# Performance work log

Measured on AMD Instinct MI355X. Metric: run time of the kernel, lower is better.

## Reference

```python
import jax, jax.numpy as jnp
import numpy as np

N_NODES = 100000
N_EDGES = 800000
N_REL = 16
D = 64
EPS = 1e-12
NEG_SLOPE = 0.01  # nn.LeakyReLU default


def _l2norm(x):
    # matches torch F.normalize(p=2, dim=-1)
    n = jnp.sqrt(jnp.sum(x * x, axis=-1, keepdims=True))
    return x / jnp.maximum(n, EPS)


def setup_inputs() -> dict:
    key = jax.random.key(0)
    ks = jax.random.split(key, 12)
    inp = {
        "src": jax.random.randint(ks[0], (N_EDGES,), 0, N_NODES, dtype=jnp.int32),
        "dst": jax.random.randint(ks[1], (N_EDGES,), 0, N_NODES, dtype=jnp.int32),
        "etype": jax.random.randint(ks[2], (N_EDGES,), 0, N_REL, dtype=jnp.int32),
        "ent_embed": jax.random.normal(ks[3], (N_NODES, D), jnp.float32) * 0.1,
        "ent_transfer": jax.random.normal(ks[4], (N_NODES, D), jnp.float32) * 0.1,
        "rel_embed": jax.random.normal(ks[5], (N_REL, D), jnp.float32) * 0.1,
        "rel_transfer": jax.random.normal(ks[6], (N_REL, D), jnp.float32) * 0.1,
        "W1_0": jax.random.normal(ks[7], (64, 32), jnp.float32) * (1.0 / np.sqrt(64)),
        "b1_0": jnp.zeros((32,), jnp.float32),
        "W2_0": jax.random.normal(ks[8], (64, 32), jnp.float32) * (1.0 / np.sqrt(64)),
        "b2_0": jnp.zeros((32,), jnp.float32),
        "W1_1": jax.random.normal(ks[9], (32, 16), jnp.float32) * (1.0 / np.sqrt(32)),
        "b1_1": jnp.zeros((16,), jnp.float32),
        "W2_1": jax.random.normal(ks[10], (32, 16), jnp.float32) * (1.0 / np.sqrt(32)),
        "b2_1": jnp.zeros((16,), jnp.float32),
    }
    return inp


def _compute_att(src, dst, etype, ent_embed, ent_transfer, rel_embed, rel_transfer):
    # per-edge gathers: h = dst node, t = src node (KGAT att_score convention)
    h_e = ent_embed[dst]          # [E, D]
    t_e = ent_embed[src]          # [E, D]
    h_p = ent_transfer[dst]
    t_p = ent_transfer[src]
    r_p = rel_transfer[etype]     # [E, D]
    r_e = rel_embed[etype]        # [E, D]
    # TransD projection + L2 normalize
    Mrt = _l2norm(t_e + jnp.sum(t_e * t_p, -1, keepdims=True) * r_p)
    Mrh = _l2norm(h_e + jnp.sum(h_e * h_p, -1, keepdims=True) * r_p)
    att = jnp.sum(Mrt * jnp.tanh(Mrh + r_e), axis=-1)  # [E]
    # edge softmax grouped by destination node
    m = jax.ops.segment_max(att, dst, num_segments=N_NODES)
    m = jnp.where(jnp.isfinite(m), m, 0.0)
    ex = jnp.exp(att - m[dst])
    s = jax.ops.segment_sum(ex, dst, num_segments=N_NODES)
    return ex / jnp.maximum(s[dst], EPS)  # [E]


def _bi_layer(node, N_h, W1, b1, W2, b2):
    out1 = jax.nn.leaky_relu((node + N_h) @ W1 + b1, NEG_SLOPE)
    out2 = jax.nn.leaky_relu((node * N_h) @ W2 + b2, NEG_SLOPE)
    return out1 + out2


def reference(src, dst, etype, ent_embed, ent_transfer, rel_embed, rel_transfer,
              W1_0, b1_0, W2_0, b2_0, W1_1, b1_1, W2_1, b2_1):
    att = _compute_att(src, dst, etype, ent_embed, ent_transfer, rel_embed, rel_transfer)
    node = ent_embed
    all_embed = [node]
    for (W1, b1, W2, b2) in [(W1_0, b1_0, W2_0, b2_0), (W1_1, b1_1, W2_1, b2_1)]:
        # u_mul_e + sum: N_h[v] = sum_{e: dst(e)=v} att_e * node[src(e)]
        msg = att[:, None] * node[src]                      # [E, d]
        N_h = jax.ops.segment_sum(msg, dst, num_segments=N_NODES)
        node = _bi_layer(node, N_h, W1, b1, W2, b2)         # dropout p=0 (eval)
        all_embed.append(_l2norm(node))
    return jnp.concatenate(all_embed, axis=1)  # [N, 64+32+16]
```

## Files before the change

kernel.cpp:

```cpp
#include <hip/hip_runtime.h>
#include <math.h>

#define EPSF 1e-12f
#define LOG2E 1.44269504f

__device__ __forceinline__ float red16(float v) {
    v += __shfl_xor(v, 1, 16);
    v += __shfl_xor(v, 2, 16);
    v += __shfl_xor(v, 4, 16);
    v += __shfl_xor(v, 8, 16);
    return v;
}

__device__ __forceinline__ float red8(float v) {
    v += __shfl_xor(v, 1, 8);
    v += __shfl_xor(v, 2, 8);
    v += __shfl_xor(v, 4, 8);
    return v;
}

__device__ __forceinline__ float fast_tanh(float x) {
    float E = __builtin_amdgcn_exp2f(x * (2.0f * LOG2E));
    return 1.0f - 2.0f * __builtin_amdgcn_rcpf(E + 1.0f);
}

__device__ __forceinline__ float inv_norm(float x) {
    return __builtin_amdgcn_rsqf(fmaxf(x, 1e-24f));
}

__device__ __forceinline__ float leaky(float x) {
    return x > 0.0f ? x : 0.01f * x;
}

__global__ __launch_bounds__(256) void prep(
    const float* __restrict__ ent, const float* __restrict__ entT,
    float* __restrict__ dot, const int* __restrict__ dst,
    int* __restrict__ deg, int N16, int E) {
    int gid = blockIdx.x * 256 + threadIdx.x;
    if (gid < N16) {
        int v = gid >> 4, lane = gid & 15;
        const float4 a = *(const float4*)(ent  + (size_t)v * 64 + lane * 4);
        const float4 b = *(const float4*)(entT + (size_t)v * 64 + lane * 4);
        float d = red16(a.x*b.x + a.y*b.y + a.z*b.z + a.w*b.w);
        if (lane == 0) dot[v] = d;
    } else {
        int e = gid - N16;
        if (e < E) atomicAdd(&deg[dst[e]], 1);
    }
}


__global__ __launch_bounds__(256) void scan_reduce(
    const int* __restrict__ deg, int* __restrict__ part, int N) {
    __shared__ int sh[256];
    int t = threadIdx.x, i = blockIdx.x * 256 + t;
    sh[t] = (i < N) ? deg[i] : 0;
    __syncthreads();
    for (int off = 128; off > 0; off >>= 1) {
        if (t < off) sh[t] += sh[t + off];
        __syncthreads();
    }
    if (t == 0) part[blockIdx.x] = sh[0];
}

__global__ __launch_bounds__(1024) void scan_part(int* __restrict__ part, int nb) {
    __shared__ int sh[1024];
    int t = threadIdx.x;
    int x = (t < nb) ? part[t] : 0;
    sh[t] = x;
    __syncthreads();
    for (int off = 1; off < 1024; off <<= 1) {
        int y = (t >= off) ? sh[t - off] : 0;
        __syncthreads();
        sh[t] += y;
        __syncthreads();
    }
    if (t < nb) part[t] = sh[t] - x;
}

__global__ __launch_bounds__(256) void scan_write(
    int* __restrict__ rowptr, const int* __restrict__ part, int N) {
    __shared__ int sh[256];
    int t = threadIdx.x, i = blockIdx.x * 256 + t;
    int x = (i < N) ? rowptr[i] : 0;
    sh[t] = x;
    __syncthreads();
    for (int off = 1; off < 256; off <<= 1) {
        int y = (t >= off) ? sh[t - off] : 0;
        __syncthreads();
        sh[t] += y;
        __syncthreads();
    }
    if (i < N) rowptr[i] = part[blockIdx.x] + sh[t] - x;
}

__global__ __launch_bounds__(256) void scatter_edges(
    const int* __restrict__ src, const int* __restrict__ dst,
    const int* __restrict__ ety, int* __restrict__ rowptr,
    int* __restrict__ spk, int E) {
    int e = blockIdx.x * 256 + threadIdx.x;
    if (e < E) {
        int slot = atomicAdd(&rowptr[dst[e]], 1);
        spk[slot] = src[e] | (ety[e] << 20);
    }
}

__global__ __launch_bounds__(256) void fused_l0(
    const int* __restrict__ rowptr, const int* __restrict__ spk,
    const float* __restrict__ ent, const float* __restrict__ dot,
    const float* __restrict__ relE, const float* __restrict__ relT,
    const float* __restrict__ W1, const float* __restrict__ b1,
    const float* __restrict__ W2, const float* __restrict__ b2,
    float* __restrict__ exatt, float* __restrict__ sinv,
    float* __restrict__ node1raw, float* __restrict__ out, int N) {
    __shared__ float al[8][68];
    __shared__ float bl[8][68];
    __shared__ float rT[16][68];
    __shared__ float rE[16][68];
    int t = threadIdx.x;

    {
        int r = t >> 4, c = (t & 15) * 4;
        *(float4*)&rT[r][c] = *(const float4*)(relT + r * 64 + c);
        *(float4*)&rE[r][c] = *(const float4*)(relE + r * 64 + c);
    }
    __syncthreads();

    int nv = t >> 5, half = (t >> 4) & 1, lane = t & 15;
    int v = blockIdx.x * 8 + nv;
    if (v >= N) return;

    int s = v ? rowptr[v - 1] : 0;
    int epos = rowptr[v];
    int deg = epos - s;
    int mid = s + ((deg + 1) >> 1);
    int hs   = half ? mid  : s;
    int hend = half ? epos : mid;

    const float4 he = *(const float4*)(ent + (size_t)v * 64 + lane * 4);
    float dh = dot[v];

    float4 macc = {0.f, 0.f, 0.f, 0.f};
    float sumex = 0.0f;

    for (int base = hs; base < hend; base += 16) {
        int rem = hend - base;
        int cnt = rem < 16 ? rem : 16;
        int mypk = spk[base + (lane < rem ? lane : rem - 1)];

        int pk0 = __shfl(mypk, 0, 16);
        int pk1 = __shfl(mypk, cnt > 1 ? 1 : 0, 16);
        float4 te0 = *(const float4*)(ent + (size_t)(pk0 & 0xFFFFF) * 64 + lane * 4);
        float  sd0 = dot[pk0 & 0xFFFFF];
        float4 te1 = *(const float4*)(ent + (size_t)(pk1 & 0xFFFFF) * 64 + lane * 4);
        float  sd1 = dot[pk1 & 0xFFFFF];

        for (int k = 0; k < cnt; k += 2) {
            float4 ta = te0, tb = te1;
            float  sa = sd0, sb = sd1;
            int rva = (pk0 >> 20) & 15;
            int rvb = (pk1 >> 20) & 15;
            bool hasb = (k + 1) < cnt;

            if (k + 2 < cnt) {
                pk0 = __shfl(mypk, k + 2, 16);
                pk1 = __shfl(mypk, (k + 3 < cnt) ? (k + 3) : (k + 2), 16);
                te0 = *(const float4*)(ent + (size_t)(pk0 & 0xFFFFF) * 64 + lane * 4);
                sd0 = dot[pk0 & 0xFFFFF];
                te1 = *(const float4*)(ent + (size_t)(pk1 & 0xFFFFF) * 64 + lane * 4);
                sd1 = dot[pk1 & 0xFFFFF];
            }

            const float4 rpa = *(const float4*)&rT[rva][lane * 4];
            const float4 rea = *(const float4*)&rE[rva][lane * 4];
            const float4 rpb = *(const float4*)&rT[rvb][lane * 4];
            const float4 reb = *(const float4*)&rE[rvb][lane * 4];

            float4 mta, mha, mtb, mhb;
            mta.x = ta.x + sa * rpa.x; mta.y = ta.y + sa * rpa.y;
            mta.z = ta.z + sa * rpa.z; mta.w = ta.w + sa * rpa.w;
            mha.x = he.x + dh * rpa.x; mha.y = he.y + dh * rpa.y;
            mha.z = he.z + dh * rpa.z; mha.w = he.w + dh * rpa.w;
            mtb.x = tb.x + sb * rpb.x; mtb.y = tb.y + sb * rpb.y;
            mtb.z = tb.z + sb * rpb.z; mtb.w = tb.w + sb * rpb.w;
            mhb.x = he.x + dh * rpb.x; mhb.y = he.y + dh * rpb.y;
            mhb.z = he.z + dh * rpb.z; mhb.w = he.w + dh * rpb.w;

            float ssta = red16(mta.x*mta.x + mta.y*mta.y + mta.z*mta.z + mta.w*mta.w);
            float ssha = red16(mha.x*mha.x + mha.y*mha.y + mha.z*mha.z + mha.w*mha.w);
            float sstb = red16(mtb.x*mtb.x + mtb.y*mtb.y + mtb.z*mtb.z + mtb.w*mtb.w);
            float sshb = red16(mhb.x*mhb.x + mhb.y*mhb.y + mhb.z*mhb.z + mhb.w*mhb.w);
            float ita = inv_norm(ssta), iha = inv_norm(ssha);
            float itb = inv_norm(sstb), ihb = inv_norm(sshb);

            float txa = fast_tanh(mha.x * iha + rea.x);
            float tya = fast_tanh(mha.y * iha + rea.y);
            float tza = fast_tanh(mha.z * iha + rea.z);
            float twa = fast_tanh(mha.w * iha + rea.w);
            float txb = fast_tanh(mhb.x * ihb + reb.x);
            float tyb = fast_tanh(mhb.y * ihb + reb.y);
            float tzb = fast_tanh(mhb.z * ihb + reb.z);
            float twb = fast_tanh(mhb.w * ihb + reb.w);

            float atta = ita * red16(mta.x*txa + mta.y*tya + mta.z*tza + mta.w*twa);
            float attb = itb * red16(mtb.x*txb + mtb.y*tyb + mtb.z*tzb + mtb.w*twb);

            float exa  = __builtin_amdgcn_exp2f(atta * LOG2E);
            float exbR = __builtin_amdgcn_exp2f(attb * LOG2E);
            float exb  = hasb ? exbR : 0.0f;

            if (lane == 0) {
                exatt[base + k] = exa;
                if (hasb) exatt[base + k + 1] = exbR;
            }
            sumex += exa + exb;
            macc.x += exa * ta.x + exb * tb.x;
            macc.y += exa * ta.y + exb * tb.y;
            macc.z += exa * ta.z + exb * tb.z;
            macc.w += exa * ta.w + exb * tb.w;
        }
    }

    sumex  += __shfl_xor(sumex,  16, 32);
    macc.x += __shfl_xor(macc.x, 16, 32);
    macc.y += __shfl_xor(macc.y, 16, 32);
    macc.z += __shfl_xor(macc.z, 16, 32);
    macc.w += __shfl_xor(macc.w, 16, 32);

    float inv = 1.0f / fmaxf(sumex, EPSF);
    if ((t & 31) == 0) sinv[v] = inv;
    macc.x *= inv; macc.y *= inv; macc.z *= inv; macc.w *= inv;

    if (!half) {
        *(float4*)(out + (size_t)v * 112 + lane * 4) = he;
        float4 av, bv;
        av.x = he.x + macc.x; av.y = he.y + macc.y;
        av.z = he.z + macc.z; av.w = he.w + macc.w;
        bv.x = he.x * macc.x; bv.y = he.y * macc.y;
        bv.z = he.z * macc.z; bv.w = he.w * macc.w;
        *(float4*)&al[nv][lane * 4] = av;
        *(float4*)&bl[nv][lane * 4] = bv;
    }

    int j = t & 31;
    float acc1 = b1[j], acc2 = b2[j];
    #pragma unroll
    for (int d = 0; d < 64; d += 4) {
        float4 a4 = *(const float4*)&al[nv][d];
        float4 b4 = *(const float4*)&bl[nv][d];
        acc1 += a4.x * W1[(d+0)*32 + j] + a4.y * W1[(d+1)*32 + j]
              + a4.z * W1[(d+2)*32 + j] + a4.w * W1[(d+3)*32 + j];
        acc2 += b4.x * W2[(d+0)*32 + j] + b4.y * W2[(d+1)*32 + j]
              + b4.z * W2[(d+2)*32 + j] + b4.w * W2[(d+3)*32 + j];
    }
    node1raw[(size_t)v * 32 + j] = leaky(acc1) + leaky(acc2);
}

__global__ __launch_bounds__(256) void fused_l1(
    const int* __restrict__ rowptr, const int* __restrict__ spk,
    const float* __restrict__ exatt, const float* __restrict__ sinv,
    const float* __restrict__ node1raw,
    const float* __restrict__ W1, const float* __restrict__ b1,
    const float* __restrict__ W2, const float* __restrict__ b2,
    float* __restrict__ out, int N) {
    __shared__ float A[16][36];
    __shared__ float B[16][36];
    int t = threadIdx.x;
    int nv = t >> 4, half = (t >> 3) & 1, lane = t & 7;
    int v = blockIdx.x * 16 + nv;
    if (v >= N) return;

    int s = v ? rowptr[v - 1] : 0;
    int epos = rowptr[v];
    int deg = epos - s;
    int mid = s + ((deg + 1) >> 1);
    int hs   = half ? mid  : s;
    int hend = half ? epos : mid;

    float4 n = *(const float4*)(node1raw + (size_t)v * 32 + lane * 4);
    float4 acc = {0.f, 0.f, 0.f, 0.f};

    for (int base = hs; base < hend; base += 8) {
        int rem = hend - base;
        int cnt = rem < 8 ? rem : 8;
        int idx = base + (lane < rem ? lane : rem - 1);
        int   mypk = spk[idx];
        float myex = exatt[idx];

        int pk0 = __shfl(mypk, 0, 8);
        int pk1 = __shfl(mypk, cnt > 1 ? 1 : 0, 8);
        float4 x0 = *(const float4*)(node1raw + (size_t)(pk0 & 0xFFFFF) * 32 + lane * 4);
        float4 x1 = *(const float4*)(node1raw + (size_t)(pk1 & 0xFFFFF) * 32 + lane * 4);

        for (int k = 0; k < cnt; k += 2) {
            float4 xa = x0, xb = x1;
            float aa = __shfl(myex, k, 8);
            float ab = __shfl(myex, (k + 1 < cnt) ? (k + 1) : k, 8);
            if (!((k + 1) < cnt)) ab = 0.0f;

            if (k + 2 < cnt) {
                pk0 = __shfl(mypk, k + 2, 8);
                pk1 = __shfl(mypk, (k + 3 < cnt) ? (k + 3) : (k + 2), 8);
                x0 = *(const float4*)(node1raw + (size_t)(pk0 & 0xFFFFF) * 32 + lane * 4);
                x1 = *(const float4*)(node1raw + (size_t)(pk1 & 0xFFFFF) * 32 + lane * 4);
            }
            acc.x += aa * xa.x + ab * xb.x;
            acc.y += aa * xa.y + ab * xb.y;
            acc.z += aa * xa.z + ab * xb.z;
            acc.w += aa * xa.w + ab * xb.w;
        }
    }
    acc.x += __shfl_xor(acc.x, 8, 16);
    acc.y += __shfl_xor(acc.y, 8, 16);
    acc.z += __shfl_xor(acc.z, 8, 16);
    acc.w += __shfl_xor(acc.w, 8, 16);

    float inv = sinv[v];
    acc.x *= inv; acc.y *= inv; acc.z *= inv; acc.w *= inv;

    float ss = red8(n.x*n.x + n.y*n.y + n.z*n.z + n.w*n.w);
    float inv1 = inv_norm(ss);

    if (!half) {
        float4 nn = {n.x*inv1, n.y*inv1, n.z*inv1, n.w*inv1};
        *(float4*)(out + (size_t)v * 112 + 64 + lane * 4) = nn;
        float4 av = {n.x + acc.x, n.y + acc.y, n.z + acc.z, n.w + acc.w};
        float4 bv = {n.x * acc.x, n.y * acc.y, n.z * acc.z, n.w * acc.w};
        *(float4*)&A[nv][lane * 4] = av;
        *(float4*)&B[nv][lane * 4] = bv;
    }

    int j = t & 15;
    float a1 = b1[j], a2 = b2[j];
    #pragma unroll
    for (int d = 0; d < 32; d += 4) {
        float4 a4 = *(const float4*)&A[nv][d];
        float4 b4 = *(const float4*)&B[nv][d];
        a1 += a4.x * W1[(d+0)*16 + j] + a4.y * W1[(d+1)*16 + j]
            + a4.z * W1[(d+2)*16 + j] + a4.w * W1[(d+3)*16 + j];
        a2 += b4.x * W2[(d+0)*16 + j] + b4.y * W2[(d+1)*16 + j]
            + b4.z * W2[(d+2)*16 + j] + b4.w * W2[(d+3)*16 + j];
    }
    float tot = leaky(a1) + leaky(a2);
    float s2 = red16(tot * tot);
    float inv2 = inv_norm(s2);
    out[(size_t)v * 112 + 96 + j] = tot * inv2;
}

extern "C" void kernel_launch(void* const* d_in, const int* in_sizes, int n_in,
                              void* d_out, int out_size, void* d_ws, size_t ws_size,
                              hipStream_t stream) {
    const int*   src  = (const int*)d_in[0];
    const int*   dst  = (const int*)d_in[1];
    const int*   ety  = (const int*)d_in[2];
    const float* ent  = (const float*)d_in[3];
    const float* entT = (const float*)d_in[4];
    const float* relE = (const float*)d_in[5];
    const float* relT = (const float*)d_in[6];
    const float* W1_0 = (const float*)d_in[7];
    const float* b1_0 = (const float*)d_in[8];
    const float* W2_0 = (const float*)d_in[9];
    const float* b2_0 = (const float*)d_in[10];
    const float* W1_1 = (const float*)d_in[11];
    const float* b1_1 = (const float*)d_in[12];
    const float* W2_1 = (const float*)d_in[13];
    const float* b2_1 = (const float*)d_in[14];
    float* out = (float*)d_out;

    const int E = in_sizes[0];
    const int N = in_sizes[3] / 64;
    const int nb = (N + 255) / 256;

    auto al256 = [](size_t x) { return (x + 255) & ~(size_t)255; };
    char* ws = (char*)d_ws;
    size_t offExatt = 0;
    size_t offS     = al256(offExatt + (size_t)E * 4);
    size_t offDot   = al256(offS + (size_t)N * 4);
    size_t offRow   = al256(offDot + (size_t)N * 4);
    size_t offSpk   = al256(offRow + (size_t)N * 4);
    size_t offPart  = al256(offSpk + (size_t)E * 4);
    size_t offN1    = al256(offPart + (size_t)nb * 4);
    float* exatt    = (float*)(ws + offExatt);
    float* sinv     = (float*)(ws + offS);
    float* dot      = (float*)(ws + offDot);
    int*   rowptr   = (int*)(ws + offRow);
    int*   spk      = (int*)(ws + offSpk);
    int*   part     = (int*)(ws + offPart);
    float* node1raw = (float*)(ws + offN1);

    hipMemsetAsync(rowptr, 0, (size_t)N * 4, stream);
    int N16 = N * 16;
    prep<<<(N16 + E + 255) / 256, 256, 0, stream>>>(ent, entT, dot, dst,
                                                    rowptr, N16, E);
    scan_reduce<<<nb, 256, 0, stream>>>(rowptr, part, N);
    scan_part<<<1, 1024, 0, stream>>>(part, nb);
    scan_write<<<nb, 256, 0, stream>>>(rowptr, part, N);
    int blkE = (E + 255) / 256;
    scatter_edges<<<blkE, 256, 0, stream>>>(src, dst, ety, rowptr, spk, E);

    fused_l0<<<(N + 7) / 8, 256, 0, stream>>>(
        rowptr, spk, ent, dot, relE, relT,
        W1_0, b1_0, W2_0, b2_0, exatt, sinv, node1raw, out, N);

    fused_l1<<<(N + 15) / 16, 256, 0, stream>>>(
        rowptr, spk, exatt, sinv, node1raw,
        W1_1, b1_1, W2_1, b2_1, out, N);
}
```

Measured before the change: 231.0 us.

## Pack src dot into edge list, use DPP reductions, stage transposed weights in LDS

The scatter step now stores each edge's source dot product next to its packed src/etype as an int2, so fused_l0 no longer does a dependent random gather of dot per edge. Shuffle-based row reductions become DPP row ops. The per-edge exp values are gathered into one lane each and written as a single coalesced store per chunk instead of serial lane-0 stores. Both MLP stages load transposed weights into LDS as float4 once per block, and the LDS padding is removed. The cost is a wider edge array (more bytes written in scatter and read in fused_l1), possible LDS bank conflicts from the removed padding, and the assumption that DPP row controls match the old xor masks.

Result: faster. 210.3 us (-9.0%).

```diff
diff --git a/kernel.cpp b/kernel.cpp
--- a/kernel.cpp
+++ b/kernel.cpp
@@ -4,19 +4,24 @@
 #define EPSF 1e-12f
 #define LOG2E 1.44269504f
 
+template <int CTRL>
+__device__ __forceinline__ float dppadd(float x) {
+    union { float f; int i; } u, r;
+    u.f = x;
+    r.i = __builtin_amdgcn_update_dpp(0, u.i, CTRL, 0xF, 0xF, false);
+    return x + r.f;
+}
 __device__ __forceinline__ float red16(float v) {
-    v += __shfl_xor(v, 1, 16);
-    v += __shfl_xor(v, 2, 16);
-    v += __shfl_xor(v, 4, 16);
-    v += __shfl_xor(v, 8, 16);
+    v = dppadd<0xB1>(v); v = dppadd<0x4E>(v);
+    v = dppadd<0x141>(v); v = dppadd<0x140>(v);
     return v;
 }
-
 __device__ __forceinline__ float red8(float v) {
-    v += __shfl_xor(v, 1, 8);
-    v += __shfl_xor(v, 2, 8);
-    v += __shfl_xor(v, 4, 8);
+    v = dppadd<0xB1>(v); v = dppadd<0x4E>(v); v = dppadd<0x141>(v);
     return v;
+}
+__device__ __forceinline__ float xor8add(float v) {
+    return dppadd<0x128>(v);
 }
 
 __device__ __forceinline__ float fast_tanh(float x) {
@@ -96,33 +101,44 @@
 
 __global__ __launch_bounds__(256) void scatter_edges(
     const int* __restrict__ src, const int* __restrict__ dst,
-    const int* __restrict__ ety, int* __restrict__ rowptr,
-    int* __restrict__ spk, int E) {
+    const int* __restrict__ ety, const float* __restrict__ dot,
+    int* __restrict__ rowptr, int2* __restrict__ spk2, int E) {
     int e = blockIdx.x * 256 + threadIdx.x;
     if (e < E) {
+        int sv = src[e];
         int slot = atomicAdd(&rowptr[dst[e]], 1);
-        spk[slot] = src[e] | (ety[e] << 20);
+        spk2[slot] = make_int2(sv | (ety[e] << 20), __float_as_int(dot[sv]));
     }
 }
 
 __global__ __launch_bounds__(256) void fused_l0(
-    const int* __restrict__ rowptr, const int* __restrict__ spk,
+    const int* __restrict__ rowptr, const int2* __restrict__ spk2,
     const float* __restrict__ ent, const float* __restrict__ dot,
     const float* __restrict__ relE, const float* __restrict__ relT,
     const float* __restrict__ W1, const float* __restrict__ b1,
     const float* __restrict__ W2, const float* __restrict__ b2,
     float* __restrict__ exatt, float* __restrict__ sinv,
     float* __restrict__ node1raw, float* __restrict__ out, int N) {
-    __shared__ float al[8][68];
-    __shared__ float bl[8][68];
-    __shared__ float rT[16][68];
-    __shared__ float rE[16][68];
+    __shared__ float  al[8][64];
+    __shared__ float  bl[8][64];
+    __shared__ float  rT[16][64];
+    __shared__ float  rE[16][64];
+    __shared__ float4 WtA[16 * 32];
+    __shared__ float4 WtB[16 * 32];
     int t = threadIdx.x;
 
     {
         int r = t >> 4, c = (t & 15) * 4;
         *(float4*)&rT[r][c] = *(const float4*)(relT + r * 64 + c);
         *(float4*)&rE[r][c] = *(const float4*)(relE + r * 64 + c);
+        int j = t & 31;
+        for (int dd = t >> 5; dd < 16; dd += 8) {
+            int d4 = dd * 4;
+            WtA[dd * 32 + j] = make_float4(W1[(d4+0)*32 + j], W1[(d4+1)*32 + j],
+                                           W1[(d4+2)*32 + j], W1[(d4+3)*32 + j]);
+            WtB[dd * 32 + j] = make_float4(W2[(d4+0)*32 + j], W2[(d4+1)*32 + j],
+                                           W2[(d4+2)*32 + j], W2[(d4+3)*32 + j]);
+        }
     }
     __syncthreads();
 
@@ -146,14 +162,15 @@
     for (int base = hs; base < hend; base += 16) {
         int rem = hend - base;
         int cnt = rem < 16 ? rem : 16;
-        int mypk = spk[base + (lane < rem ? lane : rem - 1)];
-
-        int pk0 = __shfl(mypk, 0, 16);
-        int pk1 = __shfl(mypk, cnt > 1 ? 1 : 0, 16);
+        int2 ms = spk2[base + (lane < rem ? lane : rem - 1)];
+        float myex = 0.0f;
+
+        int pk0 = __shfl(ms.x, 0, 16);
+        int pk1 = __shfl(ms.x, cnt > 1 ? 1 : 0, 16);
+        float sd0 = __int_as_float(__shfl(ms.y, 0, 16));
+        float sd1 = __int_as_float(__shfl(ms.y, cnt > 1 ? 1 : 0, 16));
         float4 te0 = *(const float4*)(ent + (size_t)(pk0 & 0xFFFFF) * 64 + lane * 4);
-        float  sd0 = dot[pk0 & 0xFFFFF];
         float4 te1 = *(const float4*)(ent + (size_t)(pk1 & 0xFFFFF) * 64 + lane * 4);
-        float  sd1 = dot[pk1 & 0xFFFFF];
 
         for (int k = 0; k < cnt; k += 2) {
             float4 ta = te0, tb = te1;
@@ -163,12 +180,13 @@
             bool hasb = (k + 1) < cnt;
 
             if (k + 2 < cnt) {
-                pk0 = __shfl(mypk, k + 2, 16);
-                pk1 = __shfl(mypk, (k + 3 < cnt) ? (k + 3) : (k + 2), 16);
+                int i2 = k + 2, i3 = (k + 3 < cnt) ? (k + 3) : (k + 2);
+                pk0 = __shfl(ms.x, i2, 16);
+                pk1 = __shfl(ms.x, i3, 16);
+                sd0 = __int_as_float(__shfl(ms.y, i2, 16));
+                sd1 = __int_as_float(__shfl(ms.y, i3, 16));
                 te0 = *(const float4*)(ent + (size_t)(pk0 & 0xFFFFF) * 64 + lane * 4);
-                sd0 = dot[pk0 & 0xFFFFF];
                 te1 = *(const float4*)(ent + (size_t)(pk1 & 0xFFFFF) * 64 + lane * 4);
-                sd1 = dot[pk1 & 0xFFFFF];
             }
 
             const float4 rpa = *(const float4*)&rT[rva][lane * 4];
@@ -209,16 +227,16 @@
             float exbR = __builtin_amdgcn_exp2f(attb * LOG2E);
             float exb  = hasb ? exbR : 0.0f;
 
-            if (lane == 0) {
-                exatt[base + k] = exa;
-                if (hasb) exatt[base + k + 1] = exbR;
-            }
+            myex = (lane == k) ? exa : myex;
+            myex = (lane == k + 1) ? exbR : myex;
+
             sumex += exa + exb;
             macc.x += exa * ta.x + exb * tb.x;
             macc.y += exa * ta.y + exb * tb.y;
             macc.z += exa * ta.z + exb * tb.z;
             macc.w += exa * ta.w + exb * tb.w;
         }
+        if (lane < cnt) exatt[base + lane] = myex;
     }
 
     sumex  += __shfl_xor(sumex,  16, 32);
@@ -245,27 +263,41 @@
     int j = t & 31;
     float acc1 = b1[j], acc2 = b2[j];
     #pragma unroll
-    for (int d = 0; d < 64; d += 4) {
-        float4 a4 = *(const float4*)&al[nv][d];
-        float4 b4 = *(const float4*)&bl[nv][d];
-        acc1 += a4.x * W1[(d+0)*32 + j] + a4.y * W1[(d+1)*32 + j]
-              + a4.z * W1[(d+2)*32 + j] + a4.w * W1[(d+3)*32 + j];
-        acc2 += b4.x * W2[(d+0)*32 + j] + b4.y * W2[(d+1)*32 + j]
-              + b4.z * W2[(d+2)*32 + j] + b4.w * W2[(d+3)*32 + j];
+    for (int dd = 0; dd < 16; ++dd) {
+        float4 a4 = *(const float4*)&al[nv][dd * 4];
+        float4 b4 = *(const float4*)&bl[nv][dd * 4];
+        float4 wa = WtA[dd * 32 + j];
+        float4 wb = WtB[dd * 32 + j];
+        acc1 += a4.x*wa.x + a4.y*wa.y + a4.z*wa.z + a4.w*wa.w;
+        acc2 += b4.x*wb.x + b4.y*wb.y + b4.z*wb.z + b4.w*wb.w;
     }
     node1raw[(size_t)v * 32 + j] = leaky(acc1) + leaky(acc2);
 }
 
 __global__ __launch_bounds__(256) void fused_l1(
-    const int* __restrict__ rowptr, const int* __restrict__ spk,
+    const int* __restrict__ rowptr, const int2* __restrict__ spk2,
     const float* __restrict__ exatt, const float* __restrict__ sinv,
     const float* __restrict__ node1raw,
     const float* __restrict__ W1, const float* __restrict__ b1,
     const float* __restrict__ W2, const float* __restrict__ b2,
     float* __restrict__ out, int N) {
-    __shared__ float A[16][36];
-    __shared__ float B[16][36];
+    __shared__ float  A[16][32];
+    __shared__ float  B[16][32];
+    __shared__ float4 WtC[8 * 16];
+    __shared__ float4 WtD[8 * 16];
     int t = threadIdx.x;
+
+    {
+        int tt = t & 127;
+        int j = tt & 15, dd = tt >> 4;
+        int d4 = dd * 4;
+        const float* W = (t < 128) ? W1 : W2;
+        float4* Wt = (t < 128) ? WtC : WtD;
+        Wt[dd * 16 + j] = make_float4(W[(d4+0)*16 + j], W[(d4+1)*16 + j],
+                                      W[(d4+2)*16 + j], W[(d4+3)*16 + j]);
+    }
+    __syncthreads();
+
     int nv = t >> 4, half = (t >> 3) & 1, lane = t & 7;
     int v = blockIdx.x * 16 + nv;
     if (v >= N) return;
@@ -284,7 +316,7 @@
         int rem = hend - base;
         int cnt = rem < 8 ? rem : 8;
         int idx = base + (lane < rem ? lane : rem - 1);
-        int   mypk = spk[idx];
+        int   mypk = spk2[idx].x;
         float myex = exatt[idx];
 
         int pk0 = __shfl(mypk, 0, 8);
@@ -310,10 +342,10 @@
             acc.w += aa * xa.w + ab * xb.w;
         }
     }
-    acc.x += __shfl_xor(acc.x, 8, 16);
-    acc.y += __shfl_xor(acc.y, 8, 16);
-    acc.z += __shfl_xor(acc.z, 8, 16);
-    acc.w += __shfl_xor(acc.w, 8, 16);
+    acc.x = xor8add(acc.x);
+    acc.y = xor8add(acc.y);
+    acc.z = xor8add(acc.z);
+    acc.w = xor8add(acc.w);
 
     float inv = sinv[v];
     acc.x *= inv; acc.y *= inv; acc.z *= inv; acc.w *= inv;
@@ -333,13 +365,13 @@
     int j = t & 15;
     float a1 = b1[j], a2 = b2[j];
     #pragma unroll
-    for (int d = 0; d < 32; d += 4) {
-        float4 a4 = *(const float4*)&A[nv][d];
-        float4 b4 = *(const float4*)&B[nv][d];
-        a1 += a4.x * W1[(d+0)*16 + j] + a4.y * W1[(d+1)*16 + j]
-            + a4.z * W1[(d+2)*16 + j] + a4.w * W1[(d+3)*16 + j];
-        a2 += b4.x * W2[(d+0)*16 + j] + b4.y * W2[(d+1)*16 + j]
-            + b4.z * W2[(d+2)*16 + j] + b4.w * W2[(d+3)*16 + j];
+    for (int dd = 0; dd < 8; ++dd) {
+        float4 a4 = *(const float4*)&A[nv][dd * 4];
+        float4 b4 = *(const float4*)&B[nv][dd * 4];
+        float4 wc = WtC[dd * 16 + j];
+        float4 wd = WtD[dd * 16 + j];
+        a1 += a4.x*wc.x + a4.y*wc.y + a4.z*wc.z + a4.w*wc.w;
+        a2 += b4.x*wd.x + b4.y*wd.y + b4.z*wd.z + b4.w*wd.w;
     }
     float tot = leaky(a1) + leaky(a2);
     float s2 = red16(tot * tot);
@@ -378,13 +410,13 @@
     size_t offDot   = al256(offS + (size_t)N * 4);
     size_t offRow   = al256(offDot + (size_t)N * 4);
     size_t offSpk   = al256(offRow + (size_t)N * 4);
-    size_t offPart  = al256(offSpk + (size_t)E * 4);
+    size_t offPart  = al256(offSpk + (size_t)E * 8);
     size_t offN1    = al256(offPart + (size_t)nb * 4);
     float* exatt    = (float*)(ws + offExatt);
     float* sinv     = (float*)(ws + offS);
     float* dot      = (float*)(ws + offDot);
     int*   rowptr   = (int*)(ws + offRow);
-    int*   spk      = (int*)(ws + offSpk);
+    int2*  spk2     = (int2*)(ws + offSpk);
     int*   part     = (int*)(ws + offPart);
     float* node1raw = (float*)(ws + offN1);
 
@@ -396,13 +428,13 @@
     scan_part<<<1, 1024, 0, stream>>>(part, nb);
     scan_write<<<nb, 256, 0, stream>>>(rowptr, part, N);
     int blkE = (E + 255) / 256;
-    scatter_edges<<<blkE, 256, 0, stream>>>(src, dst, ety, rowptr, spk, E);
+    scatter_edges<<<blkE, 256, 0, stream>>>(src, dst, ety, dot, rowptr, spk2, E);
 
     fused_l0<<<(N + 7) / 8, 256, 0, stream>>>(
-        rowptr, spk, ent, dot, relE, relT,
+        rowptr, spk2, ent, dot, relE, relT,
         W1_0, b1_0, W2_0, b2_0, exatt, sinv, node1raw, out, N);
 
     fused_l1<<<(N + 15) / 16, 256, 0, stream>>>(
-        rowptr, spk, exatt, sinv, node1raw,
+        rowptr, spk2, exatt, sinv, node1raw,
         W1_1, b1_1, W2_1, b2_1, out, N);
 }
```
